# Optimization experiments

Hardware: AMD Instinct MI355X
Metric: run time of the kernel (lower is better)

The kernel has to match this reference:

```python
import jax, jax.numpy as jnp
import numpy as np


def _filter_flow(img, filters, K):
    # img: [N, 2, H, W]; filters: [N, K*K, H, W] per-pixel adaptive kernels
    N, C, H, W = img.shape
    pad = (K - 1) // 2
    imgp = jnp.pad(img, ((0, 0), (0, 0), (pad, pad), (pad, pad)))
    # patches: [N, C*K*K, H, W], channel-major then row-major (dy, dx) --
    # matches torch F.unfold per single channel
    patches = jax.lax.conv_general_dilated_patches(
        imgp, (K, K), (1, 1), 'VALID',
        dimension_numbers=('NCHW', 'OIHW', 'NCHW'))
    patches = patches.reshape(N, C, K * K, H, W)
    return jnp.sum(patches * filters[:, None], axis=2)  # [N, 2, H, W]


def _grid(N, H, W, dtype):
    xx = jnp.broadcast_to(jnp.arange(W, dtype=dtype)[None, :], (H, W)) / max(W - 1, 1)
    yy = jnp.broadcast_to(jnp.arange(H, dtype=dtype)[:, None], (H, W)) / max(H - 1, 1)
    return jnp.broadcast_to(jnp.stack([xx, yy])[None], (N, 2, H, W))


def setup_inputs() -> dict:
    key = jax.random.key(0)
    k1, k2 = jax.random.split(key)
    N, K, H, W = 4, 11, 256, 256
    FF_AtoB = jax.random.uniform(k1, (N, K * K, H, W), dtype=jnp.float32)
    FF_BtoA = jax.random.uniform(k2, (N, K * K, H, W), dtype=jnp.float32)
    return {"FF_AtoB": FF_AtoB, "FF_BtoA": FF_BtoA, "filter_size": K}


def reference(FF_AtoB, FF_BtoA, filter_size):
    weight = 1.0
    N, C, H, W = FF_AtoB.shape
    K = filter_size
    grid = _grid(N, H, W, FF_AtoB.dtype)

    def cycle_loss(ff1, ff2):
        m = _filter_flow(grid, ff1, K)
        m = _filter_flow(m, ff2, K)
        diff = jnp.sqrt(jnp.sum((grid - m) ** 2, axis=1))  # [N, H, W]
        per_img = jnp.sum(diff, axis=(1, 2)) / (H * W)
        return jnp.sum(per_img) / N

    loss_ABA = cycle_loss(FF_AtoB, FF_BtoA)
    loss_BAB = cycle_loss(FF_BtoA, FF_AtoB)
    return (loss_ABA + loss_BAB) * weight
```

## Files before the change

kernel.cpp:

```cpp
#include <hip/hip_runtime.h>
#include <math.h>

#define NB    4
#define KF    11
#define KK    121
#define HH    256
#define WW    256
#define HW    (HH * WW)
#define PADK  5
#define TROWS 12
#define TW2   268
#define INVD  (1.0f / 255.0f)
#define RPB   2
#define GRID1 (NB * HH / RPB)

__global__ __launch_bounds__(256) void pass1_kernel(const float* __restrict__ F,
                                                    float* __restrict__ m1) {
    const int t   = threadIdx.x;
    const int n   = blockIdx.x / (HH / RPB);
    const int h0  = (blockIdx.x % (HH / RPB)) * RPB;
    const int sub = t >> 7;
    const int j   = t & 127;
    const int h   = h0 + sub;
    const int w0  = j * 2;

    const float2* fp = (const float2*)(F + (size_t)n * KK * HW + (size_t)h * WW + w0);

    float mk0[KF], mk1[KF];
#pragma unroll
    for (int kx = 0; kx < KF; ++kx) {
        int c0 = w0 + kx - PADK;
        mk0[kx] = (c0 >= 0 && c0 < WW) ? 1.0f : 0.0f;
        mk1[kx] = (c0 + 1 >= 0 && c0 + 1 < WW) ? 1.0f : 0.0f;
    }
    const float b0 = (float)(w0 - PADK) * INVD;

    float ax0 = 0, ay0 = 0, ax1 = 0, ay1 = 0;
    for (int ky = 0; ky < KF; ++ky) {
        int rr = h + ky - PADK;
        if (rr < 0 || rr >= HH) continue;
        float yv = (float)rr * INVD;
        const float2* fr = fp + (size_t)(ky * KF) * (HW / 2);
        float s0 = 0, s1 = 0;
#pragma unroll
        for (int kx = 0; kx < KF; ++kx) {
            float2 f = fr[(size_t)kx * (HW / 2)];
            float u0 = f.x * mk0[kx], u1 = f.y * mk1[kx];
            float xk = b0 + (float)kx * INVD;
            ax0 = fmaf(u0, xk, ax0);
            ax1 = fmaf(u1, xk + INVD, ax1);
            s0 += u0; s1 += u1;
        }
        ay0 = fmaf(yv, s0, ay0);
        ay1 = fmaf(yv, s1, ay1);
    }
    float2* ox = (float2*)(m1 + (size_t)n * 2 * HW + (size_t)h * WW + w0);
    float2* oy = (float2*)(m1 + (size_t)n * 2 * HW + HW + (size_t)h * WW + w0);
    *ox = make_float2(ax0, ax1);
    *oy = make_float2(ay0, ay1);
}

template <bool FUSE>
__global__ __launch_bounds__(256) void pass2_kernel(const float* __restrict__ F,
                                                    const float* __restrict__ m1in,
                                                    float* __restrict__ m1out,
                                                    float* __restrict__ partial) {
    __shared__ float tile[2 * TROWS * TW2];
    __shared__ float wsum[4];

    const int t   = threadIdx.x;
    const int n   = blockIdx.x / (HH / RPB);
    const int h0  = (blockIdx.x % (HH / RPB)) * RPB;
    const int sub = t >> 7;
    const int j   = t & 127;
    const int h   = h0 + sub;
    const int w0  = j * 2;

    const float* mbase = m1in + (size_t)n * 2 * HW;
    for (int i = t; i < 2 * TROWS * TW2; i += 256) {
        int ch  = i / (TROWS * TW2);
        int rem = i - ch * (TROWS * TW2);
        int r   = rem / TW2;
        int c   = rem - r * TW2;
        int rr  = h0 + r - PADK;
        int cc  = c - PADK;
        float v = 0.0f;
        if (rr >= 0 && rr < HH && cc >= 0 && cc < WW)
            v = mbase[(size_t)ch * HW + rr * WW + cc];
        tile[i] = v;
    }
    __syncthreads();

    const float2* fp = (const float2*)(F + (size_t)n * KK * HW + (size_t)h * WW + w0);

    float mk0[KF], mk1[KF];
#pragma unroll
    for (int kx = 0; kx < KF; ++kx) {
        int c0 = w0 + kx - PADK;
        mk0[kx] = (c0 >= 0 && c0 < WW) ? 1.0f : 0.0f;
        mk1[kx] = (c0 + 1 >= 0 && c0 + 1 < WW) ? 1.0f : 0.0f;
    }
    const float b0 = (float)(w0 - PADK) * INVD;

    float a1x0 = 0, a1y0 = 0, a1x1 = 0, a1y1 = 0;
    float a2x0 = 0, a2y0 = 0, a2x1 = 0, a2y1 = 0;

    for (int ky = 0; ky < KF; ++ky) {
        int rr = h + ky - PADK;
        if (rr < 0 || rr >= HH) continue;
        float yv = (float)rr * INVD;
        const float2* fr = fp + (size_t)(ky * KF) * (HW / 2);

        const float* tx = tile + (sub + ky) * TW2 + w0;
        const float* ty = tx + TROWS * TW2;
        float cx[12], cy[12];
#pragma unroll
        for (int q = 0; q < 6; ++q) {
            float2 vx = *(const float2*)(tx + 2 * q);
            float2 vy = *(const float2*)(ty + 2 * q);
            cx[2 * q] = vx.x; cx[2 * q + 1] = vx.y;
            cy[2 * q] = vy.x; cy[2 * q + 1] = vy.y;
        }

        float s0 = 0, s1 = 0;
#pragma unroll
        for (int kx = 0; kx < KF; ++kx) {
            float2 f = fr[(size_t)kx * (HW / 2)];
            if (FUSE) {
                float u0 = f.x * mk0[kx], u1 = f.y * mk1[kx];
                float xk = b0 + (float)kx * INVD;
                a1x0 = fmaf(u0, xk, a1x0);
                a1x1 = fmaf(u1, xk + INVD, a1x1);
                s0 += u0; s1 += u1;
            }
            a2x0 = fmaf(f.x, cx[kx], a2x0);
            a2x1 = fmaf(f.y, cx[kx + 1], a2x1);
            a2y0 = fmaf(f.x, cy[kx], a2y0);
            a2y1 = fmaf(f.y, cy[kx + 1], a2y1);
        }
        if (FUSE) {
            a1y0 = fmaf(yv, s0, a1y0);
            a1y1 = fmaf(yv, s1, a1y1);
        }
    }

    if (FUSE) {
        float2* ox = (float2*)(m1out + (size_t)n * 2 * HW + (size_t)h * WW + w0);
        float2* oy = (float2*)(m1out + (size_t)n * 2 * HW + HW + (size_t)h * WW + w0);
        *ox = make_float2(a1x0, a1x1);
        *oy = make_float2(a1y0, a1y1);
    }

    float gx = (float)w0 * INVD, gy = (float)h * INVD;
    float dx0 = gx - a2x0,        dy0 = gy - a2y0;
    float dx1 = gx + INVD - a2x1, dy1 = gy - a2y1;
    float d = sqrtf(dx0 * dx0 + dy0 * dy0) + sqrtf(dx1 * dx1 + dy1 * dy1);

#pragma unroll
    for (int off = 32; off > 0; off >>= 1) d += __shfl_down(d, off, 64);
    if ((t & 63) == 0) wsum[t >> 6] = d;
    __syncthreads();
    if (t == 0) partial[blockIdx.x] = wsum[0] + wsum[1] + wsum[2] + wsum[3];
}

__global__ __launch_bounds__(256) void finalize_kernel(const float* __restrict__ partial,
                                                       float* __restrict__ out) {
    __shared__ float wsum[4];
    int t = threadIdx.x;
    float s = partial[t] + partial[t + 256] + partial[t + 512] + partial[t + 768];
#pragma unroll
    for (int off = 32; off > 0; off >>= 1) s += __shfl_down(s, off, 64);
    if ((t & 63) == 0) wsum[t >> 6] = s;
    __syncthreads();
    if (t == 0)
        out[0] = (wsum[0] + wsum[1] + wsum[2] + wsum[3]) * (1.0f / ((float)HW * (float)NB));
}

extern "C" void kernel_launch(void* const* d_in, const int* in_sizes, int n_in,
                              void* d_out, int out_size, void* d_ws, size_t ws_size,
                              hipStream_t stream) {
    const float* FA = (const float*)d_in[0];
    const float* FB = (const float*)d_in[1];
    float* out = (float*)d_out;

    float* m1A = (float*)d_ws;
    float* m1B = m1A + (size_t)NB * 2 * HW;
    float* partial = m1B + (size_t)NB * 2 * HW;

    dim3 grid(GRID1), block(256);
    pass1_kernel<<<grid, block, 0, stream>>>(FA, m1A);
    pass2_kernel<true><<<grid, block, 0, stream>>>(FB, m1A, m1B, partial);
    pass2_kernel<false><<<grid, block, 0, stream>>>(FA, m1B, nullptr, partial + GRID1);

    finalize_kernel<<<1, block, 0, stream>>>(partial, out);
}
```

Measured before the change: 296.1 us.

## Split filter rows across wavefronts with float4 loads and shared-memory reduction

Each block now handles one image row. Its four wavefronts split the 11 filter rows, and each thread computes 4 adjacent pixels using float4 filter loads, with the 11 loads per row issued up front. Partial sums are combined through a shared-memory cross-wave reduction, and the halo tile shrinks to 11 rows. This raises memory-level parallelism and vector load width on the bandwidth-bound filter reads. In exchange it adds extra syncs and shared-memory traffic, doubles the block count, and adds launch_bounds occupancy hints.

```diff
diff --git a/kernel.cpp b/kernel.cpp
--- a/kernel.cpp
+++ b/kernel.cpp
@@ -8,153 +8,202 @@
 #define WW    256
 #define HW    (HH * WW)
 #define PADK  5
-#define TROWS 12
-#define TW2   268
 #define INVD  (1.0f / 255.0f)
-#define RPB   2
-#define GRID1 (NB * HH / RPB)
-
-__global__ __launch_bounds__(256) void pass1_kernel(const float* __restrict__ F,
-                                                    float* __restrict__ m1) {
-    const int t   = threadIdx.x;
-    const int n   = blockIdx.x / (HH / RPB);
-    const int h0  = (blockIdx.x % (HH / RPB)) * RPB;
-    const int sub = t >> 7;
-    const int j   = t & 127;
-    const int h   = h0 + sub;
-    const int w0  = j * 2;
-
-    const float2* fp = (const float2*)(F + (size_t)n * KK * HW + (size_t)h * WW + w0);
-
-    float mk0[KF], mk1[KF];
-#pragma unroll
-    for (int kx = 0; kx < KF; ++kx) {
-        int c0 = w0 + kx - PADK;
-        mk0[kx] = (c0 >= 0 && c0 < WW) ? 1.0f : 0.0f;
-        mk1[kx] = (c0 + 1 >= 0 && c0 + 1 < WW) ? 1.0f : 0.0f;
-    }
-    const float b0 = (float)(w0 - PADK) * INVD;
-
-    float ax0 = 0, ay0 = 0, ax1 = 0, ay1 = 0;
-    for (int ky = 0; ky < KF; ++ky) {
-        int rr = h + ky - PADK;
-        if (rr < 0 || rr >= HH) continue;
-        float yv = (float)rr * INVD;
-        const float2* fr = fp + (size_t)(ky * KF) * (HW / 2);
-        float s0 = 0, s1 = 0;
-#pragma unroll
-        for (int kx = 0; kx < KF; ++kx) {
-            float2 f = fr[(size_t)kx * (HW / 2)];
-            float u0 = f.x * mk0[kx], u1 = f.y * mk1[kx];
-            float xk = b0 + (float)kx * INVD;
-            ax0 = fmaf(u0, xk, ax0);
-            ax1 = fmaf(u1, xk + INVD, ax1);
-            s0 += u0; s1 += u1;
-        }
-        ay0 = fmaf(yv, s0, ay0);
-        ay1 = fmaf(yv, s1, ay1);
-    }
-    float2* ox = (float2*)(m1 + (size_t)n * 2 * HW + (size_t)h * WW + w0);
-    float2* oy = (float2*)(m1 + (size_t)n * 2 * HW + HW + (size_t)h * WW + w0);
-    *ox = make_float2(ax0, ax1);
-    *oy = make_float2(ay0, ay1);
+#define GRID_P (NB * HH)
+#define TW    268
+#define TILE_FLOATS (2 * KF * TW)
+
+
+__global__ __launch_bounds__(256, 4) void pass1_kernel(const float* __restrict__ F,
+                                                       float* __restrict__ m1) {
+    __shared__ float red[8 * 4 * 64];
+    const int t  = threadIdx.x;
+    const int n  = blockIdx.x >> 8;
+    const int h  = blockIdx.x & 255;
+    const int g  = t >> 6;
+    const int p  = t & 63;
+    const int w0 = p * 4;
+
+    float xv[14], mk[14];
+#pragma unroll
+    for (int o = 0; o < 14; ++o) {
+        int c = w0 + o - PADK;
+        bool in = (c >= 0 && c < WW);
+        mk[o] = in ? 1.0f : 0.0f;
+        xv[o] = in ? (float)c * INVD : 0.0f;
+    }
+
+    float ax[4] = {0, 0, 0, 0}, ay[4] = {0, 0, 0, 0};
+    const float* fb = F + (size_t)n * KK * HW + (size_t)h * WW + w0;
+
+#pragma unroll
+    for (int i = 0; i < 3; ++i) {
+        int ky = g + 4 * i;
+        if (ky < KF) {
+            int rr = h + ky - PADK;
+            if (rr >= 0 && rr < HH) {
+                float yv = (float)rr * INVD;
+                const float* fr = fb + (size_t)(ky * KF) * HW;
+                float4 f[KF];
+#pragma unroll
+                for (int kx = 0; kx < KF; ++kx)
+                    f[kx] = *(const float4*)(fr + (size_t)kx * HW);
+                float s[4] = {0, 0, 0, 0};
+#pragma unroll
+                for (int kx = 0; kx < KF; ++kx) {
+                    float4 fk = f[kx];
+#define TAP1(Q, FQ) \
+                    ax[Q] = fmaf(FQ, xv[kx + Q], ax[Q]); \
+                    s[Q]  = fmaf(FQ, mk[kx + Q], s[Q]);
+                    TAP1(0, fk.x) TAP1(1, fk.y) TAP1(2, fk.z) TAP1(3, fk.w)
+#undef TAP1
+                }
+#pragma unroll
+                for (int q = 0; q < 4; ++q) ay[q] = fmaf(yv, s[q], ay[q]);
+            }
+        }
+    }
+
+#pragma unroll
+    for (int q = 0; q < 4; ++q) {
+        red[(q * 4 + g) * 64 + p]       = ax[q];
+        red[((4 + q) * 4 + g) * 64 + p] = ay[q];
+    }
+    __syncthreads();
+    int q = t & 3, pp = t >> 2;
+    float vx = 0.f, vy = 0.f;
+#pragma unroll
+    for (int gg = 0; gg < 4; ++gg) {
+        vx += red[(q * 4 + gg) * 64 + pp];
+        vy += red[((4 + q) * 4 + gg) * 64 + pp];
+    }
+    float* ob = m1 + (size_t)n * 2 * HW + (size_t)h * WW;
+    ob[t]      = vx;
+    ob[HW + t] = vy;
 }
 
 template <bool FUSE>
-__global__ __launch_bounds__(256) void pass2_kernel(const float* __restrict__ F,
-                                                    const float* __restrict__ m1in,
-                                                    float* __restrict__ m1out,
-                                                    float* __restrict__ partial) {
-    __shared__ float tile[2 * TROWS * TW2];
+__global__ __launch_bounds__(256, 3) void pass2_kernel(const float* __restrict__ F,
+                                                       const float* __restrict__ m1in,
+                                                       float* __restrict__ m1out,
+                                                       float* __restrict__ partial) {
+    __shared__ float smem[TILE_FLOATS];
     __shared__ float wsum[4];
-
-    const int t   = threadIdx.x;
-    const int n   = blockIdx.x / (HH / RPB);
-    const int h0  = (blockIdx.x % (HH / RPB)) * RPB;
-    const int sub = t >> 7;
-    const int j   = t & 127;
-    const int h   = h0 + sub;
-    const int w0  = j * 2;
-
-    const float* mbase = m1in + (size_t)n * 2 * HW;
-    for (int i = t; i < 2 * TROWS * TW2; i += 256) {
-        int ch  = i / (TROWS * TW2);
-        int rem = i - ch * (TROWS * TW2);
-        int r   = rem / TW2;
-        int c   = rem - r * TW2;
-        int rr  = h0 + r - PADK;
+    const int t  = threadIdx.x;
+    const int n  = blockIdx.x >> 8;
+    const int h  = blockIdx.x & 255;
+    const int g  = t >> 6;
+    const int p  = t & 63;
+    const int w0 = p * 4;
+
+    const float* mb = m1in + (size_t)n * 2 * HW;
+    for (int i = t; i < TILE_FLOATS; i += 256) {
+        int ch  = i / (KF * TW);
+        int rem = i - ch * (KF * TW);
+        int r   = rem / TW;
+        int c   = rem - r * TW;
+        int rr  = h + r - PADK;
         int cc  = c - PADK;
         float v = 0.0f;
         if (rr >= 0 && rr < HH && cc >= 0 && cc < WW)
-            v = mbase[(size_t)ch * HW + rr * WW + cc];
-        tile[i] = v;
-    }
-    __syncthreads();
-
-    const float2* fp = (const float2*)(F + (size_t)n * KK * HW + (size_t)h * WW + w0);
-
-    float mk0[KF], mk1[KF];
-#pragma unroll
-    for (int kx = 0; kx < KF; ++kx) {
-        int c0 = w0 + kx - PADK;
-        mk0[kx] = (c0 >= 0 && c0 < WW) ? 1.0f : 0.0f;
-        mk1[kx] = (c0 + 1 >= 0 && c0 + 1 < WW) ? 1.0f : 0.0f;
-    }
-    const float b0 = (float)(w0 - PADK) * INVD;
-
-    float a1x0 = 0, a1y0 = 0, a1x1 = 0, a1y1 = 0;
-    float a2x0 = 0, a2y0 = 0, a2x1 = 0, a2y1 = 0;
-
-    for (int ky = 0; ky < KF; ++ky) {
-        int rr = h + ky - PADK;
-        if (rr < 0 || rr >= HH) continue;
-        float yv = (float)rr * INVD;
-        const float2* fr = fp + (size_t)(ky * KF) * (HW / 2);
-
-        const float* tx = tile + (sub + ky) * TW2 + w0;
-        const float* ty = tx + TROWS * TW2;
-        float cx[12], cy[12];
-#pragma unroll
-        for (int q = 0; q < 6; ++q) {
-            float2 vx = *(const float2*)(tx + 2 * q);
-            float2 vy = *(const float2*)(ty + 2 * q);
-            cx[2 * q] = vx.x; cx[2 * q + 1] = vx.y;
-            cy[2 * q] = vy.x; cy[2 * q + 1] = vy.y;
-        }
-
-        float s0 = 0, s1 = 0;
-#pragma unroll
-        for (int kx = 0; kx < KF; ++kx) {
-            float2 f = fr[(size_t)kx * (HW / 2)];
-            if (FUSE) {
-                float u0 = f.x * mk0[kx], u1 = f.y * mk1[kx];
-                float xk = b0 + (float)kx * INVD;
-                a1x0 = fmaf(u0, xk, a1x0);
-                a1x1 = fmaf(u1, xk + INVD, a1x1);
-                s0 += u0; s1 += u1;
+            v = mb[(size_t)ch * HW + rr * WW + cc];
+        smem[i] = v;
+    }
+    __syncthreads();
+
+    float xv[14], mk[14];
+    if (FUSE) {
+#pragma unroll
+        for (int o = 0; o < 14; ++o) {
+            int c = w0 + o - PADK;
+            bool in = (c >= 0 && c < WW);
+            mk[o] = in ? 1.0f : 0.0f;
+            xv[o] = in ? (float)c * INVD : 0.0f;
+        }
+    }
+
+    float a1x[4] = {0, 0, 0, 0}, a1y[4] = {0, 0, 0, 0};
+    float a2x[4] = {0, 0, 0, 0}, a2y[4] = {0, 0, 0, 0};
+    const float* fb = F + (size_t)n * KK * HW + (size_t)h * WW + w0;
+
+#pragma unroll
+    for (int i = 0; i < 3; ++i) {
+        int ky = g + 4 * i;
+        if (ky < KF) {
+            int rr = h + ky - PADK;
+            if (rr >= 0 && rr < HH) {
+                float yv = (float)rr * INVD;
+                const float* fr = fb + (size_t)(ky * KF) * HW;
+                float4 f[KF];
+#pragma unroll
+                for (int kx = 0; kx < KF; ++kx)
+                    f[kx] = *(const float4*)(fr + (size_t)kx * HW);
+
+                const float* tx = smem + ky * TW + w0;
+                const float* ty = tx + KF * TW;
+                float cx[16], cy[16];
+#pragma unroll
+                for (int u = 0; u < 4; ++u) {
+                    *(float4*)(cx + 4 * u) = *(const float4*)(tx + 4 * u);
+                    *(float4*)(cy + 4 * u) = *(const float4*)(ty + 4 * u);
+                }
+
+                float s[4] = {0, 0, 0, 0};
+#pragma unroll
+                for (int kx = 0; kx < KF; ++kx) {
+                    float4 fk = f[kx];
+#define TAP2(Q, FQ) \
+                    do { \
+                        if (FUSE) { \
+                            a1x[Q] = fmaf(FQ, xv[kx + Q], a1x[Q]); \
+                            s[Q]   = fmaf(FQ, mk[kx + Q], s[Q]); \
+                        } \
+                        a2x[Q] = fmaf(FQ, cx[kx + Q], a2x[Q]); \
+                        a2y[Q] = fmaf(FQ, cy[kx + Q], a2y[Q]); \
+                    } while (0);
+                    TAP2(0, fk.x) TAP2(1, fk.y) TAP2(2, fk.z) TAP2(3, fk.w)
+#undef TAP2
+                }
+                if (FUSE) {
+#pragma unroll
+                    for (int q = 0; q < 4; ++q) a1y[q] = fmaf(yv, s[q], a1y[q]);
+                }
             }
-            a2x0 = fmaf(f.x, cx[kx], a2x0);
-            a2x1 = fmaf(f.y, cx[kx + 1], a2x1);
-            a2y0 = fmaf(f.x, cy[kx], a2y0);
-            a2y1 = fmaf(f.y, cy[kx + 1], a2y1);
-        }
+        }
+    }
+
+    __syncthreads();
+#pragma unroll
+    for (int q = 0; q < 4; ++q) {
+        smem[(q * 4 + g) * 64 + p]        = a2x[q];
+        smem[((4 + q) * 4 + g) * 64 + p]  = a2y[q];
         if (FUSE) {
-            a1y0 = fmaf(yv, s0, a1y0);
-            a1y1 = fmaf(yv, s1, a1y1);
-        }
-    }
-
+            smem[((8 + q) * 4 + g) * 64 + p]  = a1x[q];
+            smem[((12 + q) * 4 + g) * 64 + p] = a1y[q];
+        }
+    }
+    __syncthreads();
+
+    int q = t & 3, pp = t >> 2;
+    float m2x = 0.f, m2y = 0.f, o1x = 0.f, o1y = 0.f;
+#pragma unroll
+    for (int gg = 0; gg < 4; ++gg) {
+        m2x += smem[(q * 4 + gg) * 64 + pp];
+        m2y += smem[((4 + q) * 4 + gg) * 64 + pp];
+        if (FUSE) {
+            o1x += smem[((8 + q) * 4 + gg) * 64 + pp];
+            o1y += smem[((12 + q) * 4 + gg) * 64 + pp];
+        }
+    }
     if (FUSE) {
-        float2* ox = (float2*)(m1out + (size_t)n * 2 * HW + (size_t)h * WW + w0);
-        float2* oy = (float2*)(m1out + (size_t)n * 2 * HW + HW + (size_t)h * WW + w0);
-        *ox = make_float2(a1x0, a1x1);
-        *oy = make_float2(a1y0, a1y1);
-    }
-
-    float gx = (float)w0 * INVD, gy = (float)h * INVD;
-    float dx0 = gx - a2x0,        dy0 = gy - a2y0;
-    float dx1 = gx + INVD - a2x1, dy1 = gy - a2y1;
-    float d = sqrtf(dx0 * dx0 + dy0 * dy0) + sqrtf(dx1 * dx1 + dy1 * dy1);
+        float* ob = m1out + (size_t)n * 2 * HW + (size_t)h * WW;
+        ob[t]      = o1x;
+        ob[HW + t] = o1y;
+    }
+
+    float gx = (float)t * INVD, gy = (float)h * INVD;
+    float dx = gx - m2x, dy = gy - m2y;
+    float d = sqrtf(dx * dx + dy * dy);
 
 #pragma unroll
     for (int off = 32; off > 0; off >>= 1) d += __shfl_down(d, off, 64);
@@ -167,7 +216,9 @@
                                                        float* __restrict__ out) {
     __shared__ float wsum[4];
     int t = threadIdx.x;
-    float s = partial[t] + partial[t + 256] + partial[t + 512] + partial[t + 768];
+    float s = 0.f;
+#pragma unroll
+    for (int i = 0; i < 8; ++i) s += partial[t + 256 * i];
 #pragma unroll
     for (int off = 32; off > 0; off >>= 1) s += __shfl_down(s, off, 64);
     if ((t & 63) == 0) wsum[t >> 6] = s;
@@ -187,10 +238,10 @@
     float* m1B = m1A + (size_t)NB * 2 * HW;
     float* partial = m1B + (size_t)NB * 2 * HW;
 
-    dim3 grid(GRID1), block(256);
+    dim3 grid(GRID_P), block(256);
     pass1_kernel<<<grid, block, 0, stream>>>(FA, m1A);
     pass2_kernel<true><<<grid, block, 0, stream>>>(FB, m1A, m1B, partial);
-    pass2_kernel<false><<<grid, block, 0, stream>>>(FA, m1B, nullptr, partial + GRID1);
+    pass2_kernel<false><<<grid, block, 0, stream>>>(FA, m1B, nullptr, partial + GRID_P);
 
     finalize_kernel<<<1, block, 0, stream>>>(partial, out);
 }
```

Measured after the change: 296.4 us. About the same (+0.1%).
